# Optimization experiments

Measured on AMD Instinct MI355X. Metric: run time of the kernel, lower is better.

The kernel has to match this reference:

```python
import jax, jax.numpy as jnp
import numpy as np

N = 100000  # nodes (in_features)
D = 32      # out_features
E = 1600000 # edges


def setup_inputs() -> dict:
    key = jax.random.key(0)
    k1, k2, k3, k4, k5 = jax.random.split(key, 5)
    edge_row = jax.random.randint(k1, (E,), 0, N, dtype=jnp.int64)
    edge_col = jax.random.randint(k2, (E,), 0, N, dtype=jnp.int64)
    edge_val = jax.random.uniform(k3, (E,), dtype=jnp.float32)
    weight = jax.random.normal(k4, (N, D), dtype=jnp.float32)
    bias = jax.random.normal(k5, (D,), dtype=jnp.float32)
    return {"edge_row": edge_row, "edge_col": edge_col,
            "edge_val": edge_val, "weight": weight, "bias": bias}


def reference(edge_row, edge_col, edge_val, weight, bias):
    # out = adj @ weight + bias, adj given in COO form.
    # Gather weight rows per edge column, scale by edge value,
    # segment-sum into destination rows. [E, D] intermediate.
    contrib = edge_val[:, None] * jnp.take(weight, edge_col, axis=0)
    out = jax.ops.segment_sum(contrib, edge_row, num_segments=N)
    return out + bias
```

## Files before the change

kernel.cpp:

```cpp
#include <hip/hip_runtime.h>


#define FEAT 32
#define LOG_RPB 7
#define RPB (1 << LOG_RPB)
#define COLBITS 17
#define CMASK ((1u << COLBITS) - 1)
#define BMAX 1024
#define HCHUNK 8192
#define PCHUNK 4096
#define PTHREADS 1024
#define CAPN 4096
#define CAP_MAX 32


__global__ __launch_bounds__(256) void gnn_zero(int* __restrict__ cnt, int B) {
    int i = blockIdx.x * 256 + threadIdx.x;
    if (i < B) cnt[i] = 0;
}

__global__ __launch_bounds__(256) void gnn_hist(
    const int* __restrict__ edge_row, int* __restrict__ cnt,
    int num_edges, int B) {
    __shared__ int h[BMAX];
    for (int b = threadIdx.x; b < BMAX; b += 256) h[b] = 0;
    __syncthreads();
    int e0 = blockIdx.x * HCHUNK;
    #pragma unroll
    for (int k = 0; k < HCHUNK / 256; ++k) {
        int e = e0 + k * 256 + threadIdx.x;
        if (e < num_edges) atomicAdd(&h[edge_row[e] >> LOG_RPB], 1);
    }
    __syncthreads();
    for (int b = threadIdx.x; b < B; b += 256) {
        int c = h[b];
        if (c) atomicAdd(&cnt[b], c);
    }
}

__global__ __launch_bounds__(1024) void gnn_scan(
    const int* __restrict__ cnt, int* __restrict__ startp,
    int* __restrict__ cursor, int B) {
    __shared__ int s[BMAX];
    int t = threadIdx.x;
    int v  = (t < B) ? cnt[t] : 0;
    int pv = (v + 3) & ~3;
    s[t] = pv;
    __syncthreads();
    for (int off = 1; off < BMAX; off <<= 1) {
        int u = (t >= off) ? s[t - off] : 0;
        __syncthreads();
        s[t] += u;
        __syncthreads();
    }
    if (t < B) {
        int st = s[t] - pv;
        startp[t] = st;
        cursor[t] = st;
    }
}

__global__ __launch_bounds__(PTHREADS) void gnn_part(
    const int* __restrict__ edge_row,
    const int* __restrict__ edge_col,
    const float* __restrict__ edge_val,
    int* __restrict__ cursor,
    float2* __restrict__ parts,
    int num_edges, int B) {
    __shared__ float2 lrec[PCHUNK];
    __shared__ unsigned short lbkt[PCHUNK];
    __shared__ int st[BMAX];
    __shared__ int cur[BMAX];
    __shared__ int cb[BMAX];
    int t = threadIdx.x;
    for (int b = t; b < BMAX; b += PTHREADS) cur[b] = 0;
    __syncthreads();

    int e0 = blockIdx.x * PCHUNK;
    int cnt_chunk = num_edges - e0;
    if (cnt_chunk > PCHUNK) cnt_chunk = PCHUNK;

    int rloc[PCHUNK / PTHREADS];
    #pragma unroll
    for (int k = 0; k < PCHUNK / PTHREADS; ++k) {
        int e = e0 + k * PTHREADS + t;
        rloc[k] = (e < num_edges) ? edge_row[e] : -1;
        if (rloc[k] >= 0) atomicAdd(&cur[rloc[k] >> LOG_RPB], 1);
    }
    __syncthreads();

    int v = (t < B) ? cur[t] : 0;
    st[t] = v;
    __syncthreads();
    for (int off = 1; off < BMAX; off <<= 1) {
        int u = (t >= off) ? st[t - off] : 0;
        __syncthreads();
        st[t] += u;
        __syncthreads();
    }
    st[t] -= v;
    if (t < B) {
        cur[t] = st[t];
        cb[t]  = v ? atomicAdd(&cursor[t], v) : 0;
    }
    __syncthreads();

    #pragma unroll
    for (int k = 0; k < PCHUNK / PTHREADS; ++k) {
        int e = e0 + k * PTHREADS + t;
        if (rloc[k] >= 0) {
            int r = rloc[k];
            int bb = r >> LOG_RPB;
            int slot = atomicAdd(&cur[bb], 1);
            unsigned pk = (unsigned)edge_col[e] |
                          ((unsigned)(r & (RPB - 1)) << COLBITS);
            lrec[slot] = make_float2(__uint_as_float(pk), edge_val[e]);
            lbkt[slot] = (unsigned short)bb;
        }
    }
    __syncthreads();

    for (int i = t; i < cnt_chunk; i += PTHREADS) {
        int bb = lbkt[i];
        parts[(long long)cb[bb] + (i - st[bb])] = lrec[i];
    }
}

__global__ __launch_bounds__(512) void gnn_accum(
    const float2* __restrict__ parts,
    const int* __restrict__ startp,
    const int* __restrict__ cnt,
    const float* __restrict__ weight,
    const float* __restrict__ bias,
    float* __restrict__ out,
    int n_nodes) {
    __shared__ float2 srec[CAPN];
    __shared__ int h[RPB];
    __shared__ int sc[RPB];
    __shared__ int rs[RPB + 1];
    __shared__ int cur[RPB];
    int b = blockIdx.x, t = threadIdx.x;
    int n = cnt[b];
    int m = n < CAPN ? n : CAPN;
    const float2* p = parts + startp[b];

    float2 rec[CAPN / 512];
    #pragma unroll
    for (int k = 0; k < CAPN / 512; ++k) {
        int idx = t + k * 512;
        rec[k] = (idx < m) ? p[idx] : make_float2(0.f, 0.f);
    }

    if (t < RPB) h[t] = 0;
    __syncthreads();
    #pragma unroll
    for (int k = 0; k < CAPN / 512; ++k) {
        int idx = t + k * 512;
        if (idx < m) {
            unsigned rl = (__float_as_uint(rec[k].x) >> COLBITS) & (RPB - 1);
            atomicAdd(&h[rl], 1);
        }
    }
    __syncthreads();

    if (t < RPB) sc[t] = h[t];
    __syncthreads();
    #pragma unroll
    for (int off = 1; off < RPB; off <<= 1) {
        int u = (t < RPB && t >= off) ? sc[t - off] : 0;
        __syncthreads();
        if (t < RPB) sc[t] += u;
        __syncthreads();
    }
    if (t < RPB) {
        rs[t + 1] = sc[t];
        cur[t] = sc[t] - h[t];
    }
    if (t == 0) rs[0] = 0;
    __syncthreads();

    #pragma unroll
    for (int k = 0; k < CAPN / 512; ++k) {
        int idx = t + k * 512;
        if (idx < m) {
            unsigned rl = (__float_as_uint(rec[k].x) >> COLBITS) & (RPB - 1);
            int slot = atomicAdd(&cur[rl], 1);
            srec[slot] = rec[k];
        }
    }
    __syncthreads();

    int g = t >> 5;
    int f = t & 31;
    int row0 = b << LOG_RPB;
    float bf = bias[f];
    #pragma unroll 1
    for (int rr = 0; rr < 8; ++rr) {
        int rl = (g << 3) + rr;
        int s = rs[rl], e = rs[rl + 1];
        float acc = 0.f;
        for (int j = s; j < e; j += 8) {
            #pragma unroll
            for (int k = 0; k < 8; ++k) {
                int jj = j + k;
                bool ok = jj < e;
                float2 rc = srec[ok ? jj : s];
                unsigned c = __float_as_uint(rc.x) & CMASK;
                float w = weight[c * FEAT + f];
                acc += ok ? rc.y * w : 0.f;
            }
        }
        int r = row0 + rl;
        if (r < n_nodes)
            out[(long long)r * FEAT + f] = acc + bf;
    }

    if (n > CAPN) {
        __syncthreads();
        __threadfence();
        for (int idx = CAPN + t; idx < n; idx += 512) {
            float2 rc = p[idx];
            unsigned pk = __float_as_uint(rc.x);
            int c  = (int)(pk & CMASK);
            int r  = row0 + (int)((pk >> COLBITS) & (RPB - 1));
            if (r < n_nodes) {
                const float* w = weight + (long long)c * FEAT;
                for (int ff = 0; ff < FEAT; ++ff)
                    atomicAdd(out + (long long)r * FEAT + ff, rc.y * w[ff]);
            }
        }
    }
}


__global__ __launch_bounds__(256) void gnn_init(
    const float* __restrict__ bias, float* __restrict__ out,
    int* __restrict__ cnt, int total4, int n_nodes) {
    int i = blockIdx.x * blockDim.x + threadIdx.x;
    if (i < total4) {
        float4 bb = ((const float4*)bias)[i & 7];
        ((float4*)out)[i] = bb;
    }
    if (i < n_nodes) cnt[i] = 0;
}

__global__ __launch_bounds__(256) void gnn_bin(
    const int* __restrict__ edge_row,
    const int* __restrict__ edge_col,
    const float* __restrict__ edge_val,
    const float* __restrict__ weight,
    float2* __restrict__ bins,
    int* __restrict__ cnt,
    float* __restrict__ out,
    int num_edges, int cap) {
    int e = blockIdx.x * blockDim.x + threadIdx.x;
    if (e >= num_edges) return;
    int r = edge_row[e];
    int c = edge_col[e];
    float v = edge_val[e];
    int slot = atomicAdd(&cnt[r], 1);
    if (slot < cap) {
        bins[(long long)r * cap + slot] = make_float2(__int_as_float(c), v);
    } else {
        const float* w = weight + (long long)c * FEAT;
        #pragma unroll
        for (int f = 0; f < FEAT; ++f)
            atomicAdd(out + (long long)r * FEAT + f, v * w[f]);
    }
}

__global__ __launch_bounds__(256) void gnn_gather(
    const float2* __restrict__ bins,
    const int* __restrict__ cnt,
    const float* __restrict__ weight,
    float* __restrict__ out,
    int n_nodes, int cap) {
    int g = (blockIdx.x * blockDim.x + threadIdx.x) >> 5;
    int f = threadIdx.x & (FEAT - 1);
    if (g >= n_nodes) return;
    int n = cnt[g];
    n = n < cap ? n : cap;
    const float2* b = bins + (long long)g * cap;
    float a0 = 0.f, a1 = 0.f, a2 = 0.f, a3 = 0.f;
    int j = 0;
    for (; j + 4 <= n; j += 4) {
        float2 e0 = b[j], e1 = b[j + 1], e2 = b[j + 2], e3 = b[j + 3];
        a0 += e0.y * weight[(long long)__float_as_int(e0.x) * FEAT + f];
        a1 += e1.y * weight[(long long)__float_as_int(e1.x) * FEAT + f];
        a2 += e2.y * weight[(long long)__float_as_int(e2.x) * FEAT + f];
        a3 += e3.y * weight[(long long)__float_as_int(e3.x) * FEAT + f];
    }
    for (; j < n; ++j) {
        float2 e0 = b[j];
        a0 += e0.y * weight[(long long)__float_as_int(e0.x) * FEAT + f];
    }
    out[(long long)g * FEAT + f] += (a0 + a1) + (a2 + a3);
}


__global__ __launch_bounds__(256) void gnn_init_out(
    const float* __restrict__ bias, float* __restrict__ out, int total) {
    int i = blockIdx.x * blockDim.x + threadIdx.x;
    if (i < total) out[i] = bias[i & (FEAT - 1)];
}

__global__ __launch_bounds__(256) void gnn_scatter(
    const int* __restrict__ edge_row,
    const int* __restrict__ edge_col,
    const float* __restrict__ edge_val,
    const float* __restrict__ weight,
    float* __restrict__ out,
    int num_edges) {
    long long t = (long long)blockIdx.x * blockDim.x + threadIdx.x;
    int e = (int)(t >> 5);
    int f = (int)(t & (FEAT - 1));
    if (e < num_edges) {
        int r = edge_row[e];
        int c = edge_col[e];
        atomicAdd(out + r * FEAT + f, edge_val[e] * weight[c * FEAT + f]);
    }
}

extern "C" void kernel_launch(void* const* d_in, const int* in_sizes, int n_in,
                              void* d_out, int out_size, void* d_ws, size_t ws_size,
                              hipStream_t stream) {
    const int*   edge_row = (const int*)d_in[0];
    const int*   edge_col = (const int*)d_in[1];
    const float* edge_val = (const float*)d_in[2];
    const float* weight   = (const float*)d_in[3];
    const float* bias     = (const float*)d_in[4];
    float* out = (float*)d_out;

    const int E = in_sizes[0];
    const int total = out_size;
    const int N = total / FEAT;
    const int B = (N + RPB - 1) >> LOG_RPB;

    auto align256 = [](size_t x) { return (x + 255) & ~(size_t)255; };
    size_t cnt_off    = 0;
    size_t startp_off = align256(cnt_off + (size_t)B * sizeof(int));
    size_t cursor_off = align256(startp_off + (size_t)B * sizeof(int));
    size_t parts_off  = align256(cursor_off + (size_t)B * sizeof(int));
    size_t need_v5 = parts_off + ((size_t)E + 3 * (size_t)B + 64) * sizeof(float2);

    if (B >= 1 && B <= BMAX && N <= (1 << COLBITS) && E > 0 && ws_size >= need_v5) {
        int* cnt      = (int*)((char*)d_ws + cnt_off);
        int* startp   = (int*)((char*)d_ws + startp_off);
        int* cursor   = (int*)((char*)d_ws + cursor_off);
        float2* parts = (float2*)((char*)d_ws + parts_off);

        gnn_zero<<<(B + 255) / 256, 256, 0, stream>>>(cnt, B);
        gnn_hist<<<(E + HCHUNK - 1) / HCHUNK, 256, 0, stream>>>(
            edge_row, cnt, E, B);
        gnn_scan<<<1, BMAX, 0, stream>>>(cnt, startp, cursor, B);
        gnn_part<<<(E + PCHUNK - 1) / PCHUNK, PTHREADS, 0, stream>>>(
            edge_row, edge_col, edge_val, cursor, parts, E, B);
        gnn_accum<<<B, 512, 0, stream>>>(
            parts, startp, cnt, weight, bias, out, N);
        return;
    }

    size_t cnt_bytes = align256((size_t)N * sizeof(int));
    long long cap_ll = 0;
    if (ws_size > cnt_bytes)
        cap_ll = (long long)((ws_size - cnt_bytes) / ((size_t)N * sizeof(float2)));
    int cap = (int)(cap_ll > CAP_MAX ? CAP_MAX : cap_ll);

    if (cap >= 16) {
        int* cnt = (int*)d_ws;
        float2* bins = (float2*)((char*)d_ws + cnt_bytes);
        int total4 = total / 4;
        int init_threads = total4 > N ? total4 : N;
        gnn_init<<<(init_threads + 255) / 256, 256, 0, stream>>>(
            bias, out, cnt, total4, N);
        gnn_bin<<<(E + 255) / 256, 256, 0, stream>>>(
            edge_row, edge_col, edge_val, weight, bins, cnt, out, E, cap);
        long long gthreads = (long long)N * FEAT;
        gnn_gather<<<(int)((gthreads + 255) / 256), 256, 0, stream>>>(
            bins, cnt, weight, out, N, cap);
    } else {
        gnn_init_out<<<(total + 255) / 256, 256, 0, stream>>>(bias, out, total);
        long long threads = (long long)E * FEAT;
        gnn_scatter<<<(int)((threads + 255) / 256), 256, 0, stream>>>(
            edge_row, edge_col, edge_val, weight, out, E);
    }
}
```

Before: 144.5 us.

## Replace histogram+scan with fixed-capacity buckets and a spill path

Removes the separate histogram and scan kernels by giving each row bucket a fixed capacity slot region (CAPB records), so the partition kernel writes directly at bucket*CAPB plus its atomic cursor offset. Records beyond the capacity go to a spill buffer and are added afterwards by a new atomic kernel. The partition kernel also loads row, col and val with vectorized int4/float4 loads and keeps them in registers instead of re-reading col and val. This trades two kernel launches and a pass over edge_row for a larger workspace and a possible atomic spill path when buckets overflow.

Measured after the change: 126.4 us. 1.14x faster.

```diff
diff --git a/kernel.cpp b/kernel.cpp
--- a/kernel.cpp
+++ b/kernel.cpp
@@ -7,57 +7,18 @@
 #define COLBITS 17
 #define CMASK ((1u << COLBITS) - 1)
 #define BMAX 1024
-#define HCHUNK 8192
 #define PCHUNK 4096
 #define PTHREADS 1024
-#define CAPN 4096
+#define EPT (PCHUNK / PTHREADS)
+#define CAPB 2560
 #define CAP_MAX 32
 
 
-__global__ __launch_bounds__(256) void gnn_zero(int* __restrict__ cnt, int B) {
+__global__ __launch_bounds__(256) void gnn_zero(
+    int* __restrict__ cursor, int* __restrict__ scnt, int B) {
     int i = blockIdx.x * 256 + threadIdx.x;
-    if (i < B) cnt[i] = 0;
-}
-
-__global__ __launch_bounds__(256) void gnn_hist(
-    const int* __restrict__ edge_row, int* __restrict__ cnt,
-    int num_edges, int B) {
-    __shared__ int h[BMAX];
-    for (int b = threadIdx.x; b < BMAX; b += 256) h[b] = 0;
-    __syncthreads();
-    int e0 = blockIdx.x * HCHUNK;
-    #pragma unroll
-    for (int k = 0; k < HCHUNK / 256; ++k) {
-        int e = e0 + k * 256 + threadIdx.x;
-        if (e < num_edges) atomicAdd(&h[edge_row[e] >> LOG_RPB], 1);
-    }
-    __syncthreads();
-    for (int b = threadIdx.x; b < B; b += 256) {
-        int c = h[b];
-        if (c) atomicAdd(&cnt[b], c);
-    }
-}
-
-__global__ __launch_bounds__(1024) void gnn_scan(
-    const int* __restrict__ cnt, int* __restrict__ startp,
-    int* __restrict__ cursor, int B) {
-    __shared__ int s[BMAX];
-    int t = threadIdx.x;
-    int v  = (t < B) ? cnt[t] : 0;
-    int pv = (v + 3) & ~3;
-    s[t] = pv;
-    __syncthreads();
-    for (int off = 1; off < BMAX; off <<= 1) {
-        int u = (t >= off) ? s[t - off] : 0;
-        __syncthreads();
-        s[t] += u;
-        __syncthreads();
-    }
-    if (t < B) {
-        int st = s[t] - pv;
-        startp[t] = st;
-        cursor[t] = st;
-    }
+    if (i < B) cursor[i] = 0;
+    if (i == B) *scnt = 0;
 }
 
 __global__ __launch_bounds__(PTHREADS) void gnn_part(
@@ -66,12 +27,14 @@
     const float* __restrict__ edge_val,
     int* __restrict__ cursor,
     float2* __restrict__ parts,
+    float4* __restrict__ spill,
+    int* __restrict__ scnt,
     int num_edges, int B) {
     __shared__ float2 lrec[PCHUNK];
     __shared__ unsigned short lbkt[PCHUNK];
     __shared__ int st[BMAX];
     __shared__ int cur[BMAX];
-    __shared__ int cb[BMAX];
+    __shared__ int rb[BMAX];
     int t = threadIdx.x;
     for (int b = t; b < BMAX; b += PTHREADS) cur[b] = 0;
     __syncthreads();
@@ -80,13 +43,29 @@
     int cnt_chunk = num_edges - e0;
     if (cnt_chunk > PCHUNK) cnt_chunk = PCHUNK;
 
-    int rloc[PCHUNK / PTHREADS];
-    #pragma unroll
-    for (int k = 0; k < PCHUNK / PTHREADS; ++k) {
-        int e = e0 + k * PTHREADS + t;
-        rloc[k] = (e < num_edges) ? edge_row[e] : -1;
-        if (rloc[k] >= 0) atomicAdd(&cur[rloc[k] >> LOG_RPB], 1);
-    }
+    int  r[EPT], c[EPT];
+    float vv[EPT];
+    int ebase = e0 + 4 * t;
+    if (ebase + 3 < num_edges) {
+        int4  r4 = *(const int4*)(edge_row + ebase);
+        int4  c4 = *(const int4*)(edge_col + ebase);
+        float4 v4 = *(const float4*)(edge_val + ebase);
+        r[0] = r4.x; r[1] = r4.y; r[2] = r4.z; r[3] = r4.w;
+        c[0] = c4.x; c[1] = c4.y; c[2] = c4.z; c[3] = c4.w;
+        vv[0] = v4.x; vv[1] = v4.y; vv[2] = v4.z; vv[3] = v4.w;
+    } else {
+        #pragma unroll
+        for (int k = 0; k < EPT; ++k) {
+            int e = ebase + k;
+            bool ok = e < num_edges;
+            r[k]  = ok ? edge_row[e] : -1;
+            c[k]  = ok ? edge_col[e] : 0;
+            vv[k] = ok ? edge_val[e] : 0.f;
+        }
+    }
+    #pragma unroll
+    for (int k = 0; k < EPT; ++k)
+        if (r[k] >= 0) atomicAdd(&cur[r[k] >> LOG_RPB], 1);
     __syncthreads();
 
     int v = (t < B) ? cur[t] : 0;
@@ -101,20 +80,18 @@
     st[t] -= v;
     if (t < B) {
         cur[t] = st[t];
-        cb[t]  = v ? atomicAdd(&cursor[t], v) : 0;
-    }
-    __syncthreads();
-
-    #pragma unroll
-    for (int k = 0; k < PCHUNK / PTHREADS; ++k) {
-        int e = e0 + k * PTHREADS + t;
-        if (rloc[k] >= 0) {
-            int r = rloc[k];
-            int bb = r >> LOG_RPB;
+        rb[t]  = v ? atomicAdd(&cursor[t], v) : 0;
+    }
+    __syncthreads();
+
+    #pragma unroll
+    for (int k = 0; k < EPT; ++k) {
+        if (r[k] >= 0) {
+            int bb = r[k] >> LOG_RPB;
             int slot = atomicAdd(&cur[bb], 1);
-            unsigned pk = (unsigned)edge_col[e] |
-                          ((unsigned)(r & (RPB - 1)) << COLBITS);
-            lrec[slot] = make_float2(__uint_as_float(pk), edge_val[e]);
+            unsigned pk = (unsigned)c[k] |
+                          ((unsigned)(r[k] & (RPB - 1)) << COLBITS);
+            lrec[slot] = make_float2(__uint_as_float(pk), vv[k]);
             lbkt[slot] = (unsigned short)bb;
         }
     }
@@ -122,31 +99,40 @@
 
     for (int i = t; i < cnt_chunk; i += PTHREADS) {
         int bb = lbkt[i];
-        parts[(long long)cb[bb] + (i - st[bb])] = lrec[i];
+        float2 rec = lrec[i];
+        int s = rb[bb] + (i - st[bb]);
+        if (s < CAPB) {
+            parts[(long long)bb * CAPB + s] = rec;
+        } else {
+            int si = atomicAdd(scnt, 1);
+            unsigned pk = __float_as_uint(rec.x);
+            spill[si] = make_float4(
+                __uint_as_float((unsigned)(bb << LOG_RPB) + (pk >> COLBITS)),
+                __uint_as_float(pk & CMASK), rec.y, 0.f);
+        }
     }
 }
 
 __global__ __launch_bounds__(512) void gnn_accum(
     const float2* __restrict__ parts,
-    const int* __restrict__ startp,
-    const int* __restrict__ cnt,
+    const int* __restrict__ cursor,
     const float* __restrict__ weight,
     const float* __restrict__ bias,
     float* __restrict__ out,
     int n_nodes) {
-    __shared__ float2 srec[CAPN];
+    __shared__ float2 srec[CAPB];
     __shared__ int h[RPB];
     __shared__ int sc[RPB];
     __shared__ int rs[RPB + 1];
     __shared__ int cur[RPB];
     int b = blockIdx.x, t = threadIdx.x;
-    int n = cnt[b];
-    int m = n < CAPN ? n : CAPN;
-    const float2* p = parts + startp[b];
-
-    float2 rec[CAPN / 512];
-    #pragma unroll
-    for (int k = 0; k < CAPN / 512; ++k) {
+    int n = cursor[b];
+    int m = n < CAPB ? n : CAPB;
+    const float2* p = parts + (long long)b * CAPB;
+
+    float2 rec[CAPB / 512];
+    #pragma unroll
+    for (int k = 0; k < CAPB / 512; ++k) {
         int idx = t + k * 512;
         rec[k] = (idx < m) ? p[idx] : make_float2(0.f, 0.f);
     }
@@ -154,7 +140,7 @@
     if (t < RPB) h[t] = 0;
     __syncthreads();
     #pragma unroll
-    for (int k = 0; k < CAPN / 512; ++k) {
+    for (int k = 0; k < CAPB / 512; ++k) {
         int idx = t + k * 512;
         if (idx < m) {
             unsigned rl = (__float_as_uint(rec[k].x) >> COLBITS) & (RPB - 1);
@@ -180,7 +166,7 @@
     __syncthreads();
 
     #pragma unroll
-    for (int k = 0; k < CAPN / 512; ++k) {
+    for (int k = 0; k < CAPB / 512; ++k) {
         int idx = t + k * 512;
         if (idx < m) {
             unsigned rl = (__float_as_uint(rec[k].x) >> COLBITS) & (RPB - 1);
@@ -205,30 +191,34 @@
                 int jj = j + k;
                 bool ok = jj < e;
                 float2 rc = srec[ok ? jj : s];
-                unsigned c = __float_as_uint(rc.x) & CMASK;
-                float w = weight[c * FEAT + f];
+                unsigned cc = __float_as_uint(rc.x) & CMASK;
+                float w = weight[cc * FEAT + f];
                 acc += ok ? rc.y * w : 0.f;
             }
         }
-        int r = row0 + rl;
+        int rrow = row0 + rl;
+        if (rrow < n_nodes)
+            out[(long long)rrow * FEAT + f] = acc + bf;
+    }
+}
+
+__global__ __launch_bounds__(256) void gnn_spill(
+    const float4* __restrict__ spill,
+    const int* __restrict__ scnt,
+    const float* __restrict__ weight,
+    float* __restrict__ out,
+    int n_nodes) {
+    int total = *scnt;
+    int idx = (blockIdx.x * 256 + threadIdx.x) >> 5;
+    int f = threadIdx.x & 31;
+    int stride = (gridDim.x * 256) >> 5;
+    for (; idx < total; idx += stride) {
+        float4 s = spill[idx];
+        int r = (int)__float_as_uint(s.x);
+        int c = (int)__float_as_uint(s.y);
         if (r < n_nodes)
-            out[(long long)r * FEAT + f] = acc + bf;
-    }
-
-    if (n > CAPN) {
-        __syncthreads();
-        __threadfence();
-        for (int idx = CAPN + t; idx < n; idx += 512) {
-            float2 rc = p[idx];
-            unsigned pk = __float_as_uint(rc.x);
-            int c  = (int)(pk & CMASK);
-            int r  = row0 + (int)((pk >> COLBITS) & (RPB - 1));
-            if (r < n_nodes) {
-                const float* w = weight + (long long)c * FEAT;
-                for (int ff = 0; ff < FEAT; ++ff)
-                    atomicAdd(out + (long long)r * FEAT + ff, rc.y * w[ff]);
-            }
-        }
+            atomicAdd(out + (long long)r * FEAT + f,
+                      s.z * weight[(long long)c * FEAT + f]);
     }
 }
 
@@ -337,26 +327,24 @@
     const int B = (N + RPB - 1) >> LOG_RPB;
 
     auto align256 = [](size_t x) { return (x + 255) & ~(size_t)255; };
-    size_t cnt_off    = 0;
-    size_t startp_off = align256(cnt_off + (size_t)B * sizeof(int));
-    size_t cursor_off = align256(startp_off + (size_t)B * sizeof(int));
-    size_t parts_off  = align256(cursor_off + (size_t)B * sizeof(int));
-    size_t need_v5 = parts_off + ((size_t)E + 3 * (size_t)B + 64) * sizeof(float2);
-
-    if (B >= 1 && B <= BMAX && N <= (1 << COLBITS) && E > 0 && ws_size >= need_v5) {
-        int* cnt      = (int*)((char*)d_ws + cnt_off);
-        int* startp   = (int*)((char*)d_ws + startp_off);
-        int* cursor   = (int*)((char*)d_ws + cursor_off);
-        float2* parts = (float2*)((char*)d_ws + parts_off);
-
-        gnn_zero<<<(B + 255) / 256, 256, 0, stream>>>(cnt, B);
-        gnn_hist<<<(E + HCHUNK - 1) / HCHUNK, 256, 0, stream>>>(
-            edge_row, cnt, E, B);
-        gnn_scan<<<1, BMAX, 0, stream>>>(cnt, startp, cursor, B);
+    size_t cursor_off = 0;
+    size_t scnt_off   = align256(cursor_off + (size_t)B * sizeof(int));
+    size_t spill_off  = align256(scnt_off + sizeof(int));
+    size_t parts_off  = align256(spill_off + (size_t)E * sizeof(float4));
+    size_t need_v6    = parts_off + (size_t)B * CAPB * sizeof(float2);
+
+    if (B >= 1 && B <= BMAX && N <= (1 << COLBITS) && E > 0 && ws_size >= need_v6) {
+        int*    cursor = (int*)((char*)d_ws + cursor_off);
+        int*    scnt   = (int*)((char*)d_ws + scnt_off);
+        float4* spill  = (float4*)((char*)d_ws + spill_off);
+        float2* parts  = (float2*)((char*)d_ws + parts_off);
+
+        gnn_zero<<<(B + 1 + 255) / 256, 256, 0, stream>>>(cursor, scnt, B);
         gnn_part<<<(E + PCHUNK - 1) / PCHUNK, PTHREADS, 0, stream>>>(
-            edge_row, edge_col, edge_val, cursor, parts, E, B);
+            edge_row, edge_col, edge_val, cursor, parts, spill, scnt, E, B);
         gnn_accum<<<B, 512, 0, stream>>>(
-            parts, startp, cnt, weight, bias, out, N);
+            parts, cursor, weight, bias, out, N);
+        gnn_spill<<<32, 256, 0, stream>>>(spill, scnt, weight, out, N);
         return;
     }
 
```
